# Optimization experiments

Measured on AMD Instinct MI355X. Metric: run time of the kernel, lower is better.

## Reference

```python
import jax, jax.numpy as jnp
import numpy as np

N = 50000
IN_CH = 64
HID_CH = 32
NEG_SLOPE = 0.2  # PyG GATConv default for attention LeakyReLU


def _glorot(key, shape):
    fan = shape[0] + shape[-1] if len(shape) > 1 else shape[0]
    s = jnp.sqrt(6.0 / fan)
    return jax.random.uniform(key, shape, jnp.float32, -s, s)


def setup_inputs() -> dict:
    key = jax.random.key(0)
    ks = jax.random.split(key, 20)
    x = jax.random.normal(ks[0], (N, IN_CH), jnp.float32)
    edge_index = jax.random.randint(ks[1], (2, 800000), 0, N, jnp.int64)
    dims = [(IN_CH, IN_CH), (IN_CH, HID_CH), (HID_CH, IN_CH), (IN_CH, IN_CH)]
    inp = {"x": x, "edge_index": edge_index}
    for i, (di, do) in enumerate(dims, 1):
        inp[f"w{i}"] = _glorot(ks[4 * i - 2], (di, do))
        inp[f"as{i}"] = _glorot(ks[4 * i - 1], (do,))
        inp[f"ad{i}"] = _glorot(ks[4 * i], (do,))
        inp[f"b{i}"] = jnp.zeros((do,), jnp.float32)
    return inp


def _gat_layer(x, src, dst, W, a_src, a_dst, b):
    # x: [N, di] -> h: [N, do]
    h = x @ W
    # per-edge attention logits (source + destination contributions)
    e = jax.nn.leaky_relu(h[src] @ a_src + h[dst] @ a_dst, NEG_SLOPE)  # [E]
    # numerically stable segment softmax over incoming edges per dst node
    m = jax.ops.segment_max(e, dst, num_segments=N)
    ex = jnp.exp(e - m[dst])
    denom = jax.ops.segment_sum(ex, dst, num_segments=N)
    alpha = ex / (denom[dst] + 1e-16)  # [E]
    out = jax.ops.segment_sum(alpha[:, None] * h[src], dst, num_segments=N)
    return out + b


def reference(x, edge_index, w1, as1, ad1, b1, w2, as2, ad2, b2,
              w3, as3, ad3, b3, w4, as4, ad4, b4):
    # PyG GATConv adds self-loops by default
    ar = jnp.arange(N, dtype=edge_index.dtype)
    src = jnp.concatenate([edge_index[0], ar])
    dst = jnp.concatenate([edge_index[1], ar])

    h1 = jax.nn.relu(_gat_layer(x, src, dst, w1, as1, ad1, b1))
    h = _gat_layer(h1, src, dst, w2, as2, ad2, b2)
    h3 = jax.nn.relu(h)
    h4 = jax.nn.relu(_gat_layer(h3, src, dst, w3, as3, ad3, b3))
    out = _gat_layer(h4, src, dst, w4, as4, ad4, b4)
    return (out, h)
```

## Files before the change

kernel.cpp:

```cpp
#include <hip/hip_runtime.h>
#include <hip/hip_fp16.h>
#include <math.h>

#define N_NODES 50000
#define N_EDGES 800000
#define E_TOT   850000
#define NEG_SLOPE 0.2f
#define NB_SCAN 49

__global__ void csr_init(int* deg) {
    int i = blockIdx.x * blockDim.x + threadIdx.x;
    if (i < N_NODES) deg[i] = 0;
}

__global__ void csr_degree(const int* __restrict__ dst, int* __restrict__ deg,
                           int* __restrict__ rank) {
    int e = blockIdx.x * blockDim.x + threadIdx.x;
    if (e >= E_TOT) return;
    int d = (e < N_EDGES) ? dst[e] : (e - N_EDGES);
    rank[e] = atomicAdd(&deg[d], 1);
}

__global__ void scan_p1(const int* __restrict__ deg, int* __restrict__ bsum) {
    __shared__ int red[1024];
    int i = blockIdx.x * 1024 + threadIdx.x;
    red[threadIdx.x] = (i < N_NODES) ? deg[i] : 0;
    __syncthreads();
    for (int off = 512; off >= 1; off >>= 1) {
        if (threadIdx.x < off) red[threadIdx.x] += red[threadIdx.x + off];
        __syncthreads();
    }
    if (threadIdx.x == 0) bsum[blockIdx.x] = red[0];
}

__global__ void scan_p3(const int* __restrict__ deg, const int* __restrict__ bsum,
                        int* __restrict__ offs) {
    __shared__ int s[1024];
    __shared__ int bofs;
    int i = blockIdx.x * 1024 + threadIdx.x;
    int v = (i < N_NODES) ? deg[i] : 0;
    s[threadIdx.x] = v;
    if (threadIdx.x < 64) {
        int d = (threadIdx.x < NB_SCAN) ? bsum[threadIdx.x] : 0;
        int p = d;
        for (int off = 1; off < 64; off <<= 1) {
            int u = __shfl_up(p, off, 64);
            if ((int)threadIdx.x >= off) p += u;
        }
        if ((int)threadIdx.x == (int)blockIdx.x) bofs = p - d;
        if (blockIdx.x == NB_SCAN - 1 && threadIdx.x == NB_SCAN - 1)
            offs[N_NODES] = p;
    }
    __syncthreads();
    for (int off = 1; off < 1024; off <<= 1) {
        int u = (threadIdx.x >= off) ? s[threadIdx.x - off] : 0;
        __syncthreads();
        s[threadIdx.x] += u;
        __syncthreads();
    }
    if (i < N_NODES) offs[i] = bofs + s[threadIdx.x] - v;
}

__global__ void csr_fill(const int* __restrict__ src, const int* __restrict__ dst,
                         const int* __restrict__ rank, const int* __restrict__ offs,
                         int* __restrict__ csr_src) {
    int e = blockIdx.x * blockDim.x + threadIdx.x;
    if (e >= E_TOT) return;
    int s, d;
    if (e < N_EDGES) { s = src[e]; d = dst[e]; } else { s = e - N_EDGES; d = s; }
    csr_src[offs[d] + rank[e]] = s;
}

template<int DI, int DO>
__global__ void gemm_proj(const float* __restrict__ X, const float* __restrict__ W,
                          const float* __restrict__ a_src, const float* __restrict__ a_dst,
                          __half* __restrict__ Hh, float* __restrict__ ssrc,
                          float* __restrict__ sdst) {
    const int TPN = DO / 4;
    const int NPB = 256 / TPN;
    __shared__ float sW[DI * DO];
    __shared__ float sX[NPB][DI + 1];
    const int tid = threadIdx.x;
    for (int i = tid; i < DI * DO / 4; i += 256)
        ((float4*)sW)[i] = ((const float4*)W)[i];
    const int base = blockIdx.x * NPB;
    for (int i = tid; i < NPB * DI; i += 256) {
        int r = i / DI, col = i % DI;
        int node = base + r;
        sX[r][col] = (node < N_NODES) ? X[(long)node * DI + col] : 0.0f;
    }
    __syncthreads();
    const int cq = tid % TPN;
    const int g  = tid / TPN;
    const int node = base + g;
    if (node >= N_NODES) return;
    float ax = 0.0f, ay = 0.0f, az = 0.0f, aw = 0.0f;
    const float4* sW4 = (const float4*)sW;
#pragma unroll
    for (int k = 0; k < DI; k++) {
        float xv = sX[g][k];
        float4 w4 = sW4[k * TPN + cq];
        ax = fmaf(xv, w4.x, ax); ay = fmaf(xv, w4.y, ay);
        az = fmaf(xv, w4.z, az); aw = fmaf(xv, w4.w, aw);
    }
    union { uint2 u; __half2 h2[2]; } pk;
    pk.h2[0] = __float22half2_rn(make_float2(ax, ay));
    pk.h2[1] = __float22half2_rn(make_float2(az, aw));
    ((uint2*)(Hh + (long)node * DO))[cq] = pk.u;

    float4 as4 = ((const float4*)a_src)[cq];
    float4 ad4 = ((const float4*)a_dst)[cq];
    float ps = ax * as4.x + ay * as4.y + az * as4.z + aw * as4.w;
    float pd = ax * ad4.x + ay * ad4.y + az * ad4.z + aw * ad4.w;
#pragma unroll
    for (int m = TPN / 2; m >= 1; m >>= 1) {
        ps += __shfl_xor(ps, m, TPN);
        pd += __shfl_xor(pd, m, TPN);
    }
    if (cq == 0) { ssrc[node] = ps; sdst[node] = pd; }
}

template<int DIN, int DOUT>
__global__ void gather_gemm(const __half* __restrict__ Hh_in,
                            const float* __restrict__ ssrc_in,
                            const float* __restrict__ sdst_in,
                            const int* __restrict__ offs,
                            const int* __restrict__ csr_src,
                            const float* __restrict__ bias_in,
                            int relu_o, float* __restrict__ extra_out,
                            const float* __restrict__ W2,
                            const float* __restrict__ a_src2,
                            const float* __restrict__ a_dst2,
                            __half* __restrict__ Hh_out,
                            float* __restrict__ ssrc2, float* __restrict__ sdst2) {
    const int G = DIN / 4;
    const int NPB = 256 / G;
    constexpr int LDSW = (DOUT > 0) ? DIN * DOUT : 1;
    __shared__ float sW[LDSW];
    if constexpr (DOUT > 0) {
        for (int i = threadIdx.x; i < DIN * DOUT / 4; i += 256)
            ((float4*)sW)[i] = ((const float4*)W2)[i];
        __syncthreads();
    }
    const int t = threadIdx.x;
    const int node = blockIdx.x * NPB + t / G;
    const int r = t % G;
    const bool valid = (node < N_NODES);
    const int beg = valid ? offs[node] : 0;
    const int end = valid ? offs[node + 1] : 0;
    const float sdv = valid ? sdst_in[node] : 0.0f;
    const uint2* H2 = (const uint2*)Hh_in;

    float4 acc = make_float4(0.0f, 0.0f, 0.0f, 0.0f);
    float den = 0.0f;
    for (int cb = beg; cb < end; cb += G) {
        const int cnt = min(G, end - cb);
        int s0 = 0; float ex = 0.0f;
        if (r < cnt) {
            s0 = csr_src[cb + r];
            float v = ssrc_in[s0] + sdv;
            v = (v > 0.0f) ? v : NEG_SLOPE * v;
            ex = __expf(v);
        }
        den += ex;
        int j = 0;
        for (; j + 4 <= cnt; j += 4) {
            int   sa = __shfl(s0, j,     G), sb = __shfl(s0, j + 1, G);
            int   sc = __shfl(s0, j + 2, G), sd2 = __shfl(s0, j + 3, G);
            float ea = __shfl(ex, j,     G), eb = __shfl(ex, j + 1, G);
            float ec = __shfl(ex, j + 2, G), ed = __shfl(ex, j + 3, G);
            union { uint2 u; __half2 h2[2]; } ua, ub, uc, ud;
            ua.u = H2[(long)sa * G + r];
            ub.u = H2[(long)sb * G + r];
            uc.u = H2[(long)sc * G + r];
            ud.u = H2[(long)sd2 * G + r];
            float2 a0 = __half22float2(ua.h2[0]), a1 = __half22float2(ua.h2[1]);
            float2 b0 = __half22float2(ub.h2[0]), b1 = __half22float2(ub.h2[1]);
            float2 c0 = __half22float2(uc.h2[0]), c1 = __half22float2(uc.h2[1]);
            float2 d0 = __half22float2(ud.h2[0]), d1 = __half22float2(ud.h2[1]);
            acc.x = fmaf(ea, a0.x, acc.x); acc.y = fmaf(ea, a0.y, acc.y);
            acc.z = fmaf(ea, a1.x, acc.z); acc.w = fmaf(ea, a1.y, acc.w);
            acc.x = fmaf(eb, b0.x, acc.x); acc.y = fmaf(eb, b0.y, acc.y);
            acc.z = fmaf(eb, b1.x, acc.z); acc.w = fmaf(eb, b1.y, acc.w);
            acc.x = fmaf(ec, c0.x, acc.x); acc.y = fmaf(ec, c0.y, acc.y);
            acc.z = fmaf(ec, c1.x, acc.z); acc.w = fmaf(ec, c1.y, acc.w);
            acc.x = fmaf(ed, d0.x, acc.x); acc.y = fmaf(ed, d0.y, acc.y);
            acc.z = fmaf(ed, d1.x, acc.z); acc.w = fmaf(ed, d1.y, acc.w);
        }
        for (; j < cnt; j++) {
            int   sa = __shfl(s0, j, G);
            float ea = __shfl(ex, j, G);
            union { uint2 u; __half2 h2[2]; } ua;
            ua.u = H2[(long)sa * G + r];
            float2 a0 = __half22float2(ua.h2[0]), a1 = __half22float2(ua.h2[1]);
            acc.x = fmaf(ea, a0.x, acc.x); acc.y = fmaf(ea, a0.y, acc.y);
            acc.z = fmaf(ea, a1.x, acc.z); acc.w = fmaf(ea, a1.y, acc.w);
        }
    }
#pragma unroll
    for (int m = G / 2; m >= 1; m >>= 1) den += __shfl_xor(den, m, G);

    float inv = 1.0f / (den + 1e-16f);
    float4 b4 = ((const float4*)bias_in)[r];
    float4 o;
    o.x = acc.x * inv + b4.x; o.y = acc.y * inv + b4.y;
    o.z = acc.z * inv + b4.z; o.w = acc.w * inv + b4.w;
    if (valid && extra_out) ((float4*)extra_out)[(long)node * G + r] = o;
    if (relu_o) {
        o.x = fmaxf(o.x, 0.0f); o.y = fmaxf(o.y, 0.0f);
        o.z = fmaxf(o.z, 0.0f); o.w = fmaxf(o.w, 0.0f);
    }

    if constexpr (DOUT > 0) {
        constexpr int C = DOUT / (DIN / 4);
        float acc2[C];
#pragma unroll
        for (int c = 0; c < C; c++) acc2[c] = 0.0f;
        const int cbase = r * C;
#pragma unroll
        for (int kb = 0; kb < G; kb++) {
            float4 o4;
            o4.x = __shfl(o.x, kb, G);
            o4.y = __shfl(o.y, kb, G);
            o4.z = __shfl(o.z, kb, G);
            o4.w = __shfl(o.w, kb, G);
            const float* wr = &sW[(4 * kb) * DOUT + cbase];
#pragma unroll
            for (int c = 0; c < C; c++) acc2[c] = fmaf(o4.x, wr[c], acc2[c]);
            wr += DOUT;
#pragma unroll
            for (int c = 0; c < C; c++) acc2[c] = fmaf(o4.y, wr[c], acc2[c]);
            wr += DOUT;
#pragma unroll
            for (int c = 0; c < C; c++) acc2[c] = fmaf(o4.z, wr[c], acc2[c]);
            wr += DOUT;
#pragma unroll
            for (int c = 0; c < C; c++) acc2[c] = fmaf(o4.w, wr[c], acc2[c]);
        }
        float ps = 0.0f, pd = 0.0f;
#pragma unroll
        for (int c = 0; c < C; c++) {
            ps = fmaf(acc2[c], a_src2[cbase + c], ps);
            pd = fmaf(acc2[c], a_dst2[cbase + c], pd);
        }
#pragma unroll
        for (int m = G / 2; m >= 1; m >>= 1) {
            ps += __shfl_xor(ps, m, G);
            pd += __shfl_xor(pd, m, G);
        }
        if (valid) {
            union { unsigned int u1; uint2 u2; uint4 u4; __half2 h[C / 2]; } pk;
#pragma unroll
            for (int c = 0; c < C; c += 2)
                pk.h[c / 2] = __float22half2_rn(make_float2(acc2[c], acc2[c + 1]));
            char* dp = (char*)(Hh_out + (long)node * DOUT + cbase);
            if constexpr (C == 2) *(unsigned int*)dp = pk.u1;
            else if constexpr (C == 4) *(uint2*)dp = pk.u2;
            else                        *(uint4*)dp = pk.u4;
            if (r == 0) { ssrc2[node] = ps; sdst2[node] = pd; }
        }
    }
}

extern "C" void kernel_launch(void* const* d_in, const int* in_sizes, int n_in,
                              void* d_out, int out_size, void* d_ws, size_t ws_size,
                              hipStream_t stream) {
    const float* x  = (const float*)d_in[0];
    const int*   ei = (const int*)d_in[1];

    const float* w1  = (const float*)d_in[2];
    const float* as1 = (const float*)d_in[3];
    const float* ad1 = (const float*)d_in[4];
    const float* b1  = (const float*)d_in[5];
    const float* w2  = (const float*)d_in[6];
    const float* as2 = (const float*)d_in[7];
    const float* ad2 = (const float*)d_in[8];
    const float* b2  = (const float*)d_in[9];
    const float* w3  = (const float*)d_in[10];
    const float* as3 = (const float*)d_in[11];
    const float* ad3 = (const float*)d_in[12];
    const float* b3  = (const float*)d_in[13];
    const float* w4  = (const float*)d_in[14];
    const float* as4 = (const float*)d_in[15];
    const float* ad4 = (const float*)d_in[16];
    const float* b4  = (const float*)d_in[17];

    float* out_final = (float*)d_out;
    float* out_h     = (float*)d_out + N_NODES * 64;

    float* ws    = (float*)d_ws;
    __half* Hh_a = (__half*)ws;
    __half* Hh_b = (__half*)(ws + N_NODES * 32);
    float* SS_a  = ws + 2 * N_NODES * 32;
    float* SD_a  = SS_a + N_NODES;
    float* SS_b  = SD_a + N_NODES;
    float* SD_b  = SS_b + N_NODES;
    int* deg     = (int*)(SD_b + N_NODES);
    int* rank    = deg + N_NODES;
    int* offs    = rank + E_TOT;
    int* csr_src = offs + N_NODES + 1;
    int* bsum    = csr_src + E_TOT;

    const int* src = ei;
    const int* dst = ei + N_EDGES;

    csr_init<<<(N_NODES + 255) / 256, 256, 0, stream>>>(deg);
    csr_degree<<<(E_TOT + 255) / 256, 256, 0, stream>>>(dst, deg, rank);
    scan_p1<<<NB_SCAN, 1024, 0, stream>>>(deg, bsum);
    scan_p3<<<NB_SCAN, 1024, 0, stream>>>(deg, bsum, offs);
    csr_fill<<<(E_TOT + 255) / 256, 256, 0, stream>>>(src, dst, rank, offs, csr_src);

    gemm_proj<64, 64><<<(N_NODES + 15) / 16, 256, 0, stream>>>(
        x, w1, as1, ad1, Hh_a, SS_a, SD_a);

    gather_gemm<64, 32><<<(N_NODES * 16 + 255) / 256, 256, 0, stream>>>(
        Hh_a, SS_a, SD_a, offs, csr_src, b1, 1, nullptr,
        w2, as2, ad2, Hh_b, SS_b, SD_b);
    gather_gemm<32, 64><<<(N_NODES * 8 + 255) / 256, 256, 0, stream>>>(
        Hh_b, SS_b, SD_b, offs, csr_src, b2, 1, out_h,
        w3, as3, ad3, Hh_a, SS_a, SD_a);
    gather_gemm<64, 64><<<(N_NODES * 16 + 255) / 256, 256, 0, stream>>>(
        Hh_a, SS_a, SD_a, offs, csr_src, b3, 1, nullptr,
        w4, as4, ad4, Hh_b, SS_b, SD_b);
    gather_gemm<64, 0><<<(N_NODES * 16 + 255) / 256, 256, 0, stream>>>(
        Hh_b, SS_b, SD_b, offs, csr_src, b4, 0, out_final,
        nullptr, nullptr, nullptr, nullptr, nullptr, nullptr);
}
```

Baseline: 279.9 us.

## Split CSR by source range and run gathers as two-pass persistent grid

Each destination's edge list is split into two buckets by source index (below or above 25000), so the scan covers twice as many segments. The 64-wide gather layers become persistent kernels with a fixed 1024-block grid, and each thread group walks all its nodes once per source half. The goal is to keep the working set of gathered feature rows smaller per pass for better cache hit rate. The degree counting and first projection GEMM are also merged into one launch. The cost is a more complex scan, repeated per-node offset loads, and register arrays with launch bounds that may affect occupancy.

```diff
diff --git a/kernel.cpp b/kernel.cpp
--- a/kernel.cpp
+++ b/kernel.cpp
@@ -6,25 +6,78 @@
 #define N_EDGES 800000
 #define E_TOT   850000
 #define NEG_SLOPE 0.2f
-#define NB_SCAN 49
-
-__global__ void csr_init(int* deg) {
+#define SRC_SPLIT 25000
+#define N2 (2 * N_NODES)
+#define NB2 98
+#define DEG_BLOCKS ((E_TOT + 255) / 256)
+#define GEMM_BLOCKS ((N_NODES + 15) / 16)
+
+__global__ void csr_init(int* deg2) {
     int i = blockIdx.x * blockDim.x + threadIdx.x;
-    if (i < N_NODES) deg[i] = 0;
-}
-
-__global__ void csr_degree(const int* __restrict__ dst, int* __restrict__ deg,
-                           int* __restrict__ rank) {
-    int e = blockIdx.x * blockDim.x + threadIdx.x;
-    if (e >= E_TOT) return;
-    int d = (e < N_EDGES) ? dst[e] : (e - N_EDGES);
-    rank[e] = atomicAdd(&deg[d], 1);
-}
-
-__global__ void scan_p1(const int* __restrict__ deg, int* __restrict__ bsum) {
+    if (i < N2) deg2[i] = 0;
+}
+
+__global__ void degree_gemm(const int* __restrict__ src, const int* __restrict__ dst,
+                            int* __restrict__ deg2, int* __restrict__ rank,
+                            const float* __restrict__ X, const float* __restrict__ W,
+                            const float* __restrict__ a_src, const float* __restrict__ a_dst,
+                            __half* __restrict__ Hh, float* __restrict__ ssrc,
+                            float* __restrict__ sdst) {
+    __shared__ float sW[64 * 64];
+    __shared__ float sX[16][65];
+    if (blockIdx.x < DEG_BLOCKS) {
+        int e = blockIdx.x * 256 + threadIdx.x;
+        if (e >= E_TOT) return;
+        int s, d;
+        if (e < N_EDGES) { s = src[e]; d = dst[e]; } else { s = e - N_EDGES; d = s; }
+        int rng = (s >= SRC_SPLIT) ? 1 : 0;
+        rank[e] = atomicAdd(&deg2[2 * d + rng], 1);
+        return;
+    }
+    const int bx = blockIdx.x - DEG_BLOCKS;
+    const int tid = threadIdx.x;
+    for (int i = tid; i < 64 * 64 / 4; i += 256)
+        ((float4*)sW)[i] = ((const float4*)W)[i];
+    const int base = bx * 16;
+    for (int i = tid; i < 16 * 64; i += 256) {
+        int r = i / 64, col = i % 64;
+        int node = base + r;
+        sX[r][col] = (node < N_NODES) ? X[(long)node * 64 + col] : 0.0f;
+    }
+    __syncthreads();
+    const int cq = tid % 16;
+    const int g  = tid / 16;
+    const int node = base + g;
+    if (node >= N_NODES) return;
+    float ax = 0.0f, ay = 0.0f, az = 0.0f, aw = 0.0f;
+    const float4* sW4 = (const float4*)sW;
+#pragma unroll
+    for (int k = 0; k < 64; k++) {
+        float xv = sX[g][k];
+        float4 w4 = sW4[k * 16 + cq];
+        ax = fmaf(xv, w4.x, ax); ay = fmaf(xv, w4.y, ay);
+        az = fmaf(xv, w4.z, az); aw = fmaf(xv, w4.w, aw);
+    }
+    union { uint2 u; __half2 h2[2]; } pk;
+    pk.h2[0] = __float22half2_rn(make_float2(ax, ay));
+    pk.h2[1] = __float22half2_rn(make_float2(az, aw));
+    ((uint2*)(Hh + (long)node * 64))[cq] = pk.u;
+    float4 as4 = ((const float4*)a_src)[cq];
+    float4 ad4 = ((const float4*)a_dst)[cq];
+    float ps = ax * as4.x + ay * as4.y + az * as4.z + aw * as4.w;
+    float pd = ax * ad4.x + ay * ad4.y + az * ad4.z + aw * ad4.w;
+#pragma unroll
+    for (int m = 8; m >= 1; m >>= 1) {
+        ps += __shfl_xor(ps, m, 16);
+        pd += __shfl_xor(pd, m, 16);
+    }
+    if (cq == 0) { ssrc[node] = ps; sdst[node] = pd; }
+}
+
+__global__ void scan_p1(const int* __restrict__ deg2, int* __restrict__ bsum) {
     __shared__ int red[1024];
     int i = blockIdx.x * 1024 + threadIdx.x;
-    red[threadIdx.x] = (i < N_NODES) ? deg[i] : 0;
+    red[threadIdx.x] = (i < N2) ? deg2[i] : 0;
     __syncthreads();
     for (int off = 512; off >= 1; off >>= 1) {
         if (threadIdx.x < off) red[threadIdx.x] += red[threadIdx.x + off];
@@ -33,98 +86,49 @@
     if (threadIdx.x == 0) bsum[blockIdx.x] = red[0];
 }
 
-__global__ void scan_p3(const int* __restrict__ deg, const int* __restrict__ bsum,
-                        int* __restrict__ offs) {
+__global__ void scan_p3(const int* __restrict__ deg2, const int* __restrict__ bsum,
+                        int* __restrict__ offs2) {
     __shared__ int s[1024];
-    __shared__ int bofs;
+    __shared__ int sb[128];
     int i = blockIdx.x * 1024 + threadIdx.x;
-    int v = (i < N_NODES) ? deg[i] : 0;
+    int v = (i < N2) ? deg2[i] : 0;
     s[threadIdx.x] = v;
-    if (threadIdx.x < 64) {
-        int d = (threadIdx.x < NB_SCAN) ? bsum[threadIdx.x] : 0;
-        int p = d;
-        for (int off = 1; off < 64; off <<= 1) {
-            int u = __shfl_up(p, off, 64);
-            if ((int)threadIdx.x >= off) p += u;
-        }
-        if ((int)threadIdx.x == (int)blockIdx.x) bofs = p - d;
-        if (blockIdx.x == NB_SCAN - 1 && threadIdx.x == NB_SCAN - 1)
-            offs[N_NODES] = p;
-    }
+    if (threadIdx.x < 128) sb[threadIdx.x] = (threadIdx.x < NB2) ? bsum[threadIdx.x] : 0;
     __syncthreads();
+    for (int off = 1; off < 128; off <<= 1) {
+        int u = (threadIdx.x < 128 && threadIdx.x >= off) ? sb[threadIdx.x - off] : 0;
+        __syncthreads();
+        if (threadIdx.x < 128) sb[threadIdx.x] += u;
+        __syncthreads();
+    }
+    if (blockIdx.x == NB2 - 1 && threadIdx.x == 0) offs2[N2] = sb[NB2 - 1];
+    const int bofs = (blockIdx.x == 0) ? 0 : sb[blockIdx.x - 1];
     for (int off = 1; off < 1024; off <<= 1) {
         int u = (threadIdx.x >= off) ? s[threadIdx.x - off] : 0;
         __syncthreads();
         s[threadIdx.x] += u;
         __syncthreads();
     }
-    if (i < N_NODES) offs[i] = bofs + s[threadIdx.x] - v;
+    if (i < N2) offs2[i] = bofs + s[threadIdx.x] - v;
 }
 
 __global__ void csr_fill(const int* __restrict__ src, const int* __restrict__ dst,
-                         const int* __restrict__ rank, const int* __restrict__ offs,
+                         const int* __restrict__ rank, const int* __restrict__ offs2,
                          int* __restrict__ csr_src) {
     int e = blockIdx.x * blockDim.x + threadIdx.x;
     if (e >= E_TOT) return;
     int s, d;
     if (e < N_EDGES) { s = src[e]; d = dst[e]; } else { s = e - N_EDGES; d = s; }
-    csr_src[offs[d] + rank[e]] = s;
-}
-
-template<int DI, int DO>
-__global__ void gemm_proj(const float* __restrict__ X, const float* __restrict__ W,
-                          const float* __restrict__ a_src, const float* __restrict__ a_dst,
-                          __half* __restrict__ Hh, float* __restrict__ ssrc,
-                          float* __restrict__ sdst) {
-    const int TPN = DO / 4;
-    const int NPB = 256 / TPN;
-    __shared__ float sW[DI * DO];
-    __shared__ float sX[NPB][DI + 1];
-    const int tid = threadIdx.x;
-    for (int i = tid; i < DI * DO / 4; i += 256)
-        ((float4*)sW)[i] = ((const float4*)W)[i];
-    const int base = blockIdx.x * NPB;
-    for (int i = tid; i < NPB * DI; i += 256) {
-        int r = i / DI, col = i % DI;
-        int node = base + r;
-        sX[r][col] = (node < N_NODES) ? X[(long)node * DI + col] : 0.0f;
-    }
-    __syncthreads();
-    const int cq = tid % TPN;
-    const int g  = tid / TPN;
-    const int node = base + g;
-    if (node >= N_NODES) return;
-    float ax = 0.0f, ay = 0.0f, az = 0.0f, aw = 0.0f;
-    const float4* sW4 = (const float4*)sW;
-#pragma unroll
-    for (int k = 0; k < DI; k++) {
-        float xv = sX[g][k];
-        float4 w4 = sW4[k * TPN + cq];
-        ax = fmaf(xv, w4.x, ax); ay = fmaf(xv, w4.y, ay);
-        az = fmaf(xv, w4.z, az); aw = fmaf(xv, w4.w, aw);
-    }
-    union { uint2 u; __half2 h2[2]; } pk;
-    pk.h2[0] = __float22half2_rn(make_float2(ax, ay));
-    pk.h2[1] = __float22half2_rn(make_float2(az, aw));
-    ((uint2*)(Hh + (long)node * DO))[cq] = pk.u;
-
-    float4 as4 = ((const float4*)a_src)[cq];
-    float4 ad4 = ((const float4*)a_dst)[cq];
-    float ps = ax * as4.x + ay * as4.y + az * as4.z + aw * as4.w;
-    float pd = ax * ad4.x + ay * ad4.y + az * ad4.z + aw * ad4.w;
-#pragma unroll
-    for (int m = TPN / 2; m >= 1; m >>= 1) {
-        ps += __shfl_xor(ps, m, TPN);
-        pd += __shfl_xor(pd, m, TPN);
-    }
-    if (cq == 0) { ssrc[node] = ps; sdst[node] = pd; }
-}
-
-template<int DIN, int DOUT>
+    int rng = (s >= SRC_SPLIT) ? 1 : 0;
+    csr_src[offs2[2 * d + rng] + rank[e]] = s;
+}
+
+template<int DIN, int DOUT, int PASSES>
+__launch_bounds__(256, 4)
 __global__ void gather_gemm(const __half* __restrict__ Hh_in,
                             const float* __restrict__ ssrc_in,
                             const float* __restrict__ sdst_in,
-                            const int* __restrict__ offs,
+                            const int* __restrict__ offs2,
                             const int* __restrict__ csr_src,
                             const float* __restrict__ bias_in,
                             int relu_o, float* __restrict__ extra_out,
@@ -133,8 +137,10 @@
                             const float* __restrict__ a_dst2,
                             __half* __restrict__ Hh_out,
                             float* __restrict__ ssrc2, float* __restrict__ sdst2) {
-    const int G = DIN / 4;
-    const int NPB = 256 / G;
+    constexpr int G = DIN / 4;
+    constexpr int GPB = 256 / G;
+    constexpr int NG = 1024 * GPB;
+    constexpr int ITER = (N_NODES + NG - 1) / NG;
     constexpr int LDSW = (DOUT > 0) ? DIN * DOUT : 1;
     __shared__ float sW[LDSW];
     if constexpr (DOUT > 0) {
@@ -142,122 +148,148 @@
             ((float4*)sW)[i] = ((const float4*)W2)[i];
         __syncthreads();
     }
-    const int t = threadIdx.x;
-    const int node = blockIdx.x * NPB + t / G;
-    const int r = t % G;
-    const bool valid = (node < N_NODES);
-    const int beg = valid ? offs[node] : 0;
-    const int end = valid ? offs[node + 1] : 0;
-    const float sdv = valid ? sdst_in[node] : 0.0f;
+    const int gid = blockIdx.x * GPB + threadIdx.x / G;
+    const int r = threadIdx.x % G;
     const uint2* H2 = (const uint2*)Hh_in;
 
-    float4 acc = make_float4(0.0f, 0.0f, 0.0f, 0.0f);
-    float den = 0.0f;
-    for (int cb = beg; cb < end; cb += G) {
-        const int cnt = min(G, end - cb);
-        int s0 = 0; float ex = 0.0f;
-        if (r < cnt) {
-            s0 = csr_src[cb + r];
-            float v = ssrc_in[s0] + sdv;
-            v = (v > 0.0f) ? v : NEG_SLOPE * v;
-            ex = __expf(v);
+    float4 acc[ITER];
+    float  den[ITER];
+    float  sdv[ITER];
+#pragma unroll
+    for (int it = 0; it < ITER; it++) {
+        acc[it] = make_float4(0.0f, 0.0f, 0.0f, 0.0f);
+        den[it] = 0.0f;
+        int node = gid + it * NG;
+        sdv[it] = (node < N_NODES) ? sdst_in[node] : 0.0f;
+    }
+
+#pragma unroll
+    for (int p = 0; p < PASSES; p++) {
+#pragma unroll
+        for (int it = 0; it < ITER; it++) {
+            const int node = gid + it * NG;
+            if (node >= N_NODES) continue;
+            int rbeg, rend;
+            if constexpr (PASSES == 2) {
+                rbeg = offs2[2 * node + p];
+                rend = offs2[2 * node + p + 1];
+            } else {
+                rbeg = offs2[2 * node];
+                rend = offs2[2 * node + 2];
+            }
+            const float sdvv = sdv[it];
+            for (int cb = rbeg; cb < rend; cb += G) {
+                const int cnt = min(G, rend - cb);
+                int s0 = 0; float ex = 0.0f;
+                if (r < cnt) {
+                    s0 = csr_src[cb + r];
+                    float v = ssrc_in[s0] + sdvv;
+                    v = (v > 0.0f) ? v : NEG_SLOPE * v;
+                    ex = __expf(v);
+                }
+                den[it] += ex;
+                int j = 0;
+                for (; j + 4 <= cnt; j += 4) {
+                    int   sa = __shfl(s0, j,     G), sb = __shfl(s0, j + 1, G);
+                    int   sc = __shfl(s0, j + 2, G), sd2 = __shfl(s0, j + 3, G);
+                    float ea = __shfl(ex, j,     G), eb = __shfl(ex, j + 1, G);
+                    float ec = __shfl(ex, j + 2, G), ed = __shfl(ex, j + 3, G);
+                    union { uint2 u; __half2 h2[2]; } ua, ub, uc, ud;
+                    ua.u = H2[(long)sa * G + r];
+                    ub.u = H2[(long)sb * G + r];
+                    uc.u = H2[(long)sc * G + r];
+                    ud.u = H2[(long)sd2 * G + r];
+                    float2 a0 = __half22float2(ua.h2[0]), a1 = __half22float2(ua.h2[1]);
+                    float2 b0 = __half22float2(ub.h2[0]), b1 = __half22float2(ub.h2[1]);
+                    float2 c0 = __half22float2(uc.h2[0]), c1 = __half22float2(uc.h2[1]);
+                    float2 d0 = __half22float2(ud.h2[0]), d1 = __half22float2(ud.h2[1]);
+                    acc[it].x = fmaf(ea, a0.x, acc[it].x); acc[it].y = fmaf(ea, a0.y, acc[it].y);
+                    acc[it].z = fmaf(ea, a1.x, acc[it].z); acc[it].w = fmaf(ea, a1.y, acc[it].w);
+                    acc[it].x = fmaf(eb, b0.x, acc[it].x); acc[it].y = fmaf(eb, b0.y, acc[it].y);
+                    acc[it].z = fmaf(eb, b1.x, acc[it].z); acc[it].w = fmaf(eb, b1.y, acc[it].w);
+                    acc[it].x = fmaf(ec, c0.x, acc[it].x); acc[it].y = fmaf(ec, c0.y, acc[it].y);
+                    acc[it].z = fmaf(ec, c1.x, acc[it].z); acc[it].w = fmaf(ec, c1.y, acc[it].w);
+                    acc[it].x = fmaf(ed, d0.x, acc[it].x); acc[it].y = fmaf(ed, d0.y, acc[it].y);
+                    acc[it].z = fmaf(ed, d1.x, acc[it].z); acc[it].w = fmaf(ed, d1.y, acc[it].w);
+                }
+                for (; j < cnt; j++) {
+                    int   sa = __shfl(s0, j, G);
+                    float ea = __shfl(ex, j, G);
+                    union { uint2 u; __half2 h2[2]; } ua;
+                    ua.u = H2[(long)sa * G + r];
+                    float2 a0 = __half22float2(ua.h2[0]), a1 = __half22float2(ua.h2[1]);
+                    acc[it].x = fmaf(ea, a0.x, acc[it].x); acc[it].y = fmaf(ea, a0.y, acc[it].y);
+                    acc[it].z = fmaf(ea, a1.x, acc[it].z); acc[it].w = fmaf(ea, a1.y, acc[it].w);
+                }
+            }
         }
-        den += ex;
-        int j = 0;
-        for (; j + 4 <= cnt; j += 4) {
-            int   sa = __shfl(s0, j,     G), sb = __shfl(s0, j + 1, G);
-            int   sc = __shfl(s0, j + 2, G), sd2 = __shfl(s0, j + 3, G);
-            float ea = __shfl(ex, j,     G), eb = __shfl(ex, j + 1, G);
-            float ec = __shfl(ex, j + 2, G), ed = __shfl(ex, j + 3, G);
-            union { uint2 u; __half2 h2[2]; } ua, ub, uc, ud;
-            ua.u = H2[(long)sa * G + r];
-            ub.u = H2[(long)sb * G + r];
-            uc.u = H2[(long)sc * G + r];
-            ud.u = H2[(long)sd2 * G + r];
-            float2 a0 = __half22float2(ua.h2[0]), a1 = __half22float2(ua.h2[1]);
-            float2 b0 = __half22float2(ub.h2[0]), b1 = __half22float2(ub.h2[1]);
-            float2 c0 = __half22float2(uc.h2[0]), c1 = __half22float2(uc.h2[1]);
-            float2 d0 = __half22float2(ud.h2[0]), d1 = __half22float2(ud.h2[1]);
-            acc.x = fmaf(ea, a0.x, acc.x); acc.y = fmaf(ea, a0.y, acc.y);
-            acc.z = fmaf(ea, a1.x, acc.z); acc.w = fmaf(ea, a1.y, acc.w);
-            acc.x = fmaf(eb, b0.x, acc.x); acc.y = fmaf(eb, b0.y, acc.y);
-            acc.z = fmaf(eb, b1.x, acc.z); acc.w = fmaf(eb, b1.y, acc.w);
-            acc.x = fmaf(ec, c0.x, acc.x); acc.y = fmaf(ec, c0.y, acc.y);
-            acc.z = fmaf(ec, c1.x, acc.z); acc.w = fmaf(ec, c1.y, acc.w);
-            acc.x = fmaf(ed, d0.x, acc.x); acc.y = fmaf(ed, d0.y, acc.y);
-            acc.z = fmaf(ed, d1.x, acc.z); acc.w = fmaf(ed, d1.y, acc.w);
+    }
+
+#pragma unroll
+    for (int it = 0; it < ITER; it++) {
+        const int node = gid + it * NG;
+        const bool valid = (node < N_NODES);
+        float dn = den[it];
+#pragma unroll
+        for (int m = G / 2; m >= 1; m >>= 1) dn += __shfl_xor(dn, m, G);
+        float inv = 1.0f / (dn + 1e-16f);
+        float4 b4 = ((const float4*)bias_in)[r];
+        float4 o;
+        o.x = acc[it].x * inv + b4.x; o.y = acc[it].y * inv + b4.y;
+        o.z = acc[it].z * inv + b4.z; o.w = acc[it].w * inv + b4.w;
+        if (valid && extra_out) ((float4*)extra_out)[(long)node * G + r] = o;
+        if (relu_o) {
+            o.x = fmaxf(o.x, 0.0f); o.y = fmaxf(o.y, 0.0f);
+            o.z = fmaxf(o.z, 0.0f); o.w = fmaxf(o.w, 0.0f);
         }
-        for (; j < cnt; j++) {
-            int   sa = __shfl(s0, j, G);
-            float ea = __shfl(ex, j, G);
-            union { uint2 u; __half2 h2[2]; } ua;
-            ua.u = H2[(long)sa * G + r];
-            float2 a0 = __half22float2(ua.h2[0]), a1 = __half22float2(ua.h2[1]);
-            acc.x = fmaf(ea, a0.x, acc.x); acc.y = fmaf(ea, a0.y, acc.y);
-            acc.z = fmaf(ea, a1.x, acc.z); acc.w = fmaf(ea, a1.y, acc.w);
-        }
-    }
-#pragma unroll
-    for (int m = G / 2; m >= 1; m >>= 1) den += __shfl_xor(den, m, G);
-
-    float inv = 1.0f / (den + 1e-16f);
-    float4 b4 = ((const float4*)bias_in)[r];
-    float4 o;
-    o.x = acc.x * inv + b4.x; o.y = acc.y * inv + b4.y;
-    o.z = acc.z * inv + b4.z; o.w = acc.w * inv + b4.w;
-    if (valid && extra_out) ((float4*)extra_out)[(long)node * G + r] = o;
-    if (relu_o) {
-        o.x = fmaxf(o.x, 0.0f); o.y = fmaxf(o.y, 0.0f);
-        o.z = fmaxf(o.z, 0.0f); o.w = fmaxf(o.w, 0.0f);
-    }
-
-    if constexpr (DOUT > 0) {
-        constexpr int C = DOUT / (DIN / 4);
-        float acc2[C];
-#pragma unroll
-        for (int c = 0; c < C; c++) acc2[c] = 0.0f;
-        const int cbase = r * C;
-#pragma unroll
-        for (int kb = 0; kb < G; kb++) {
-            float4 o4;
-            o4.x = __shfl(o.x, kb, G);
-            o4.y = __shfl(o.y, kb, G);
-            o4.z = __shfl(o.z, kb, G);
-            o4.w = __shfl(o.w, kb, G);
-            const float* wr = &sW[(4 * kb) * DOUT + cbase];
-#pragma unroll
-            for (int c = 0; c < C; c++) acc2[c] = fmaf(o4.x, wr[c], acc2[c]);
-            wr += DOUT;
-#pragma unroll
-            for (int c = 0; c < C; c++) acc2[c] = fmaf(o4.y, wr[c], acc2[c]);
-            wr += DOUT;
-#pragma unroll
-            for (int c = 0; c < C; c++) acc2[c] = fmaf(o4.z, wr[c], acc2[c]);
-            wr += DOUT;
-#pragma unroll
-            for (int c = 0; c < C; c++) acc2[c] = fmaf(o4.w, wr[c], acc2[c]);
-        }
-        float ps = 0.0f, pd = 0.0f;
-#pragma unroll
-        for (int c = 0; c < C; c++) {
-            ps = fmaf(acc2[c], a_src2[cbase + c], ps);
-            pd = fmaf(acc2[c], a_dst2[cbase + c], pd);
-        }
-#pragma unroll
-        for (int m = G / 2; m >= 1; m >>= 1) {
-            ps += __shfl_xor(ps, m, G);
-            pd += __shfl_xor(pd, m, G);
-        }
-        if (valid) {
-            union { unsigned int u1; uint2 u2; uint4 u4; __half2 h[C / 2]; } pk;
-#pragma unroll
-            for (int c = 0; c < C; c += 2)
-                pk.h[c / 2] = __float22half2_rn(make_float2(acc2[c], acc2[c + 1]));
-            char* dp = (char*)(Hh_out + (long)node * DOUT + cbase);
-            if constexpr (C == 2) *(unsigned int*)dp = pk.u1;
-            else if constexpr (C == 4) *(uint2*)dp = pk.u2;
-            else                        *(uint4*)dp = pk.u4;
-            if (r == 0) { ssrc2[node] = ps; sdst2[node] = pd; }
+        if constexpr (DOUT > 0) {
+            constexpr int C = DOUT / G;
+            float acc2[C];
+#pragma unroll
+            for (int c = 0; c < C; c++) acc2[c] = 0.0f;
+            const int cbase = r * C;
+#pragma unroll
+            for (int kb = 0; kb < G; kb++) {
+                float4 o4;
+                o4.x = __shfl(o.x, kb, G);
+                o4.y = __shfl(o.y, kb, G);
+                o4.z = __shfl(o.z, kb, G);
+                o4.w = __shfl(o.w, kb, G);
+                const float* wr = &sW[(4 * kb) * DOUT + cbase];
+#pragma unroll
+                for (int c = 0; c < C; c++) acc2[c] = fmaf(o4.x, wr[c], acc2[c]);
+                wr += DOUT;
+#pragma unroll
+                for (int c = 0; c < C; c++) acc2[c] = fmaf(o4.y, wr[c], acc2[c]);
+                wr += DOUT;
+#pragma unroll
+                for (int c = 0; c < C; c++) acc2[c] = fmaf(o4.z, wr[c], acc2[c]);
+                wr += DOUT;
+#pragma unroll
+                for (int c = 0; c < C; c++) acc2[c] = fmaf(o4.w, wr[c], acc2[c]);
+            }
+            float ps = 0.0f, pd = 0.0f;
+#pragma unroll
+            for (int c = 0; c < C; c++) {
+                ps = fmaf(acc2[c], a_src2[cbase + c], ps);
+                pd = fmaf(acc2[c], a_dst2[cbase + c], pd);
+            }
+#pragma unroll
+            for (int m = G / 2; m >= 1; m >>= 1) {
+                ps += __shfl_xor(ps, m, G);
+                pd += __shfl_xor(pd, m, G);
+            }
+            if (valid) {
+                union { unsigned int u1; uint2 u2; uint4 u4; __half2 h[C / 2]; } pk;
+#pragma unroll
+                for (int c = 0; c < C; c += 2)
+                    pk.h[c / 2] = __float22half2_rn(make_float2(acc2[c], acc2[c + 1]));
+                char* dp = (char*)(Hh_out + (long)node * DOUT + cbase);
+                if constexpr (C == 2) *(unsigned int*)dp = pk.u1;
+                else if constexpr (C == 4) *(uint2*)dp = pk.u2;
+                else                        *(uint4*)dp = pk.u4;
+                if (r == 0) { ssrc2[node] = ps; sdst2[node] = pd; }
+            }
         }
     }
 }
@@ -295,34 +327,32 @@
     float* SD_a  = SS_a + N_NODES;
     float* SS_b  = SD_a + N_NODES;
     float* SD_b  = SS_b + N_NODES;
-    int* deg     = (int*)(SD_b + N_NODES);
-    int* rank    = deg + N_NODES;
-    int* offs    = rank + E_TOT;
-    int* csr_src = offs + N_NODES + 1;
+    int* deg2    = (int*)(SD_b + N_NODES);
+    int* rank    = deg2 + N2;
+    int* offs2   = rank + E_TOT;
+    int* csr_src = offs2 + N2 + 1;
     int* bsum    = csr_src + E_TOT;
 
     const int* src = ei;
     const int* dst = ei + N_EDGES;
 
-    csr_init<<<(N_NODES + 255) / 256, 256, 0, stream>>>(deg);
-    csr_degree<<<(E_TOT + 255) / 256, 256, 0, stream>>>(dst, deg, rank);
-    scan_p1<<<NB_SCAN, 1024, 0, stream>>>(deg, bsum);
-    scan_p3<<<NB_SCAN, 1024, 0, stream>>>(deg, bsum, offs);
-    csr_fill<<<(E_TOT + 255) / 256, 256, 0, stream>>>(src, dst, rank, offs, csr_src);
-
-    gemm_proj<64, 64><<<(N_NODES + 15) / 16, 256, 0, stream>>>(
-        x, w1, as1, ad1, Hh_a, SS_a, SD_a);
-
-    gather_gemm<64, 32><<<(N_NODES * 16 + 255) / 256, 256, 0, stream>>>(
-        Hh_a, SS_a, SD_a, offs, csr_src, b1, 1, nullptr,
+    csr_init<<<(N2 + 255) / 256, 256, 0, stream>>>(deg2);
+    degree_gemm<<<DEG_BLOCKS + GEMM_BLOCKS, 256, 0, stream>>>(
+        src, dst, deg2, rank, x, w1, as1, ad1, Hh_a, SS_a, SD_a);
+    scan_p1<<<NB2, 1024, 0, stream>>>(deg2, bsum);
+    scan_p3<<<NB2, 1024, 0, stream>>>(deg2, bsum, offs2);
+    csr_fill<<<(E_TOT + 255) / 256, 256, 0, stream>>>(src, dst, rank, offs2, csr_src);
+
+    gather_gemm<64, 32, 2><<<1024, 256, 0, stream>>>(
+        Hh_a, SS_a, SD_a, offs2, csr_src, b1, 1, nullptr,
         w2, as2, ad2, Hh_b, SS_b, SD_b);
-    gather_gemm<32, 64><<<(N_NODES * 8 + 255) / 256, 256, 0, stream>>>(
-        Hh_b, SS_b, SD_b, offs, csr_src, b2, 1, out_h,
+    gather_gemm<32, 64, 1><<<1024, 256, 0, stream>>>(
+        Hh_b, SS_b, SD_b, offs2, csr_src, b2, 1, out_h,
         w3, as3, ad3, Hh_a, SS_a, SD_a);
-    gather_gemm<64, 64><<<(N_NODES * 16 + 255) / 256, 256, 0, stream>>>(
-        Hh_a, SS_a, SD_a, offs, csr_src, b3, 1, nullptr,
+    gather_gemm<64, 64, 2><<<1024, 256, 0, stream>>>(
+        Hh_a, SS_a, SD_a, offs2, csr_src, b3, 1, nullptr,
         w4, as4, ad4, Hh_b, SS_b, SD_b);
-    gather_gemm<64, 0><<<(N_NODES * 16 + 255) / 256, 256, 0, stream>>>(
-        Hh_b, SS_b, SD_b, offs, csr_src, b4, 0, out_final,
+    gather_gemm<64, 0, 2><<<1024, 256, 0, stream>>>(
+        Hh_b, SS_b, SD_b, offs2, csr_src, b4, 0, out_final,
         nullptr, nullptr, nullptr, nullptr, nullptr, nullptr);
 }
```

Result: slower. 306.0 us (+9.3%).
